# Kernel optimization log

Measured on AMD Instinct MI355X. Metric: run time of the kernel, lower is better.

## Reference

```python
import jax, jax.numpy as jnp
import numpy as np

S = 3000    # number of candidate spans (rows of g_i)
P = 80000   # total (mention, antecedent) pairs
GI = 768    # gi_dim
DD = 20     # distance/genre/speaker embedding dim
HID = 150   # mlp hidden dim (fixed in source)
ORDER = 2   # N: one higher-order refinement pass


def setup_inputs() -> dict:
    key = jax.random.key(0)
    ks = jax.random.split(key, 18)
    gij = 3 * GI + 3 * DD
    g_i = jax.random.normal(ks[0], (S, GI), jnp.float32)
    mention_scores = jax.random.normal(ks[1], (S, 1), jnp.float32)
    # sorted segment ids: ragged antecedent counts per mention, grouped contiguously
    mention_ids = jnp.sort(jax.random.randint(ks[2], (P,), 0, S, dtype=jnp.int32))
    antecedent_ids = jax.random.randint(ks[3], (P,), 0, S, dtype=jnp.int32)
    dist_bins = jax.random.randint(ks[4], (P,), 0, 10, dtype=jnp.int32)
    genre_ids = jax.random.randint(ks[5], (P,), 0, 7, dtype=jnp.int32) + 1   # 1..7, 0 is padding_idx
    speaker_ids = jax.random.randint(ks[6], (P,), 0, 2, dtype=jnp.int32) + 1  # 1..2, 0 is padding_idx
    w = lambda k, shp: 0.02 * jax.random.normal(k, shp, jnp.float32)
    dist_emb = w(ks[7], (10, DD))
    genre_emb = w(ks[8], (8, DD)).at[0].set(0.0)     # padding_idx=0
    speaker_emb = w(ks[9], (3, DD)).at[0].set(0.0)   # padding_idx=0
    W1 = w(ks[10], (gij, HID)); b1 = jnp.zeros((HID,), jnp.float32)
    W2 = w(ks[11], (HID, HID)); b2 = jnp.zeros((HID,), jnp.float32)
    W3 = w(ks[12], (HID, 1)); b3 = jnp.zeros((1,), jnp.float32)
    Wf = w(ks[13], (2 * GI, 1)); bf = jnp.zeros((1,), jnp.float32)
    return {"g_i": g_i, "mention_scores": mention_scores, "mention_ids": mention_ids,
            "antecedent_ids": antecedent_ids, "dist_bins": dist_bins, "genre_ids": genre_ids,
            "speaker_ids": speaker_ids, "dist_emb": dist_emb, "genre_emb": genre_emb,
            "speaker_emb": speaker_emb, "W1": W1, "b1": b1, "W2": W2, "b2": b2,
            "W3": W3, "b3": b3, "Wf": Wf, "bf": bf}


def _mlp(x, W1, b1, W2, b2, W3, b3):
    h = jax.nn.relu(x @ W1 + b1)
    h = jax.nn.relu(h @ W2 + b2)
    return h @ W3 + b3


def reference(g_i, mention_scores, mention_ids, antecedent_ids, dist_bins, genre_ids,
              speaker_ids, dist_emb, genre_emb, speaker_emb, W1, b1, W2, b2, W3, b3, Wf, bf):
    phi = jnp.concatenate([dist_emb[dist_bins], genre_emb[genre_ids], speaker_emb[speaker_ids]], axis=1)  # [P,60]
    seg = dict(num_segments=S, indices_are_sorted=True)
    g = g_i
    scores = None
    for n in range(ORDER):
        i_g = g[mention_ids]                # [P,GI] gather
        j_g = g[antecedent_ids]             # [P,GI] gather
        pairs = jnp.concatenate([i_g, j_g, i_g * j_g, phi], axis=1)  # [P,gij]
        scores = _mlp(pairs, W1, b1, W2, b2, W3, b3)                 # [P,1]
        if n < ORDER - 1:
            # higher_order_refinement: ragged segment softmax + weighted scatter update
            s = scores[:, 0]
            seg_max = jax.ops.segment_max(s, mention_ids, **seg)
            safe_max = jnp.where(jnp.isfinite(seg_max), seg_max, 0.0)
            e = jnp.exp(s - safe_max[mention_ids])
            denom = jax.ops.segment_sum(e, mention_ids, **seg)
            attn = e / jnp.where(denom > 0, denom, 1.0)[mention_ids]
            weighted = jax.ops.segment_sum(attn[:, None] * j_g, mention_ids, **seg)  # [S,GI]
            counts = jax.ops.segment_sum(jnp.ones_like(s), mention_ids, **seg)
            f = jax.nn.sigmoid(jnp.concatenate([g, weighted], axis=1) @ Wf + bf)  # [S,1]
            # NOTE: faithful to the source bug: f * mention_id (the integer index), not f * mention_g
            ids_f = jnp.arange(S, dtype=g.dtype)[:, None]
            g_new = f * ids_f + (1.0 - f) * weighted
            g = jnp.where(counts[:, None] > 0, g_new, g)
    s_i = mention_scores[mention_ids]
    s_j = mention_scores[antecedent_ids]
    coref_scores = s_i + s_j + scores       # [P,1]
    # segment softmax with an extra epsilon (score 0) logit per mention
    c = coref_scores[:, 0]
    seg_max = jax.ops.segment_max(c, mention_ids, **seg)
    m = jnp.maximum(jnp.where(jnp.isfinite(seg_max), seg_max, 0.0), 0.0)  # include epsilon logit 0
    e = jnp.exp(c - m[mention_ids])
    denom = jax.ops.segment_sum(e, mention_ids, **seg) + jnp.exp(-m)
    pair_probs = e / denom[mention_ids]     # [P]
    eps_probs = jnp.exp(-m) / denom         # [S]
    return coref_scores, pair_probs, eps_probs
```

## Files before the change

kernel.cpp:

```cpp
#include <hip/hip_runtime.h>

#define GI   768
#define HID  150
#define HPAD 160
#define DDIM 20

typedef __attribute__((ext_vector_type(8))) short v8s;
typedef __attribute__((ext_vector_type(4))) float f32x4;

#define MFMA16(A, B, C) __builtin_amdgcn_mfma_f32_16x16x32_bf16(A, B, C, 0, 0, 0)

__device__ __forceinline__ ushort bf16rn(float x) {
  unsigned u = __float_as_uint(x);
  return (ushort)((u + 0x7fffu + ((u >> 16) & 1u)) >> 16);
}
__device__ __forceinline__ float b2f(ushort u) {
  return __uint_as_float((unsigned)u << 16);
}
__device__ __forceinline__ void tsplit(float x, ushort& h, ushort& l) {
  unsigned u = __float_as_uint(x);
  h = (ushort)(u >> 16);
  float d = x - __uint_as_float(u & 0xffff0000u);
  l = (ushort)(__float_as_uint(d) >> 16);
}
__device__ __forceinline__ uint4 pack8(const ushort* v) {
  uint4 r;
  r.x = v[0] | ((unsigned)v[1] << 16); r.y = v[2] | ((unsigned)v[3] << 16);
  r.z = v[4] | ((unsigned)v[5] << 16); r.w = v[6] | ((unsigned)v[7] << 16);
  return r;
}
__device__ __forceinline__ v8s mk8(const ushort* v) {
  union { uint4 u; v8s s; } t;
  t.u = pack8(v);
  return t.s;
}

__global__ void seg_kernel(const int* __restrict__ mI, int* __restrict__ segs,
                           int P, int S) {
  int m = blockIdx.x * 256 + threadIdx.x;
  if (m > S) return;
  int lo = 0, hi = P;
  while (lo < hi) { int mid = (lo + hi) >> 1; if (mI[mid] < m) lo = mid + 1; else hi = mid; }
  segs[m] = lo;
}

__global__ void phi_kernel(const float* __restrict__ de, const float* __restrict__ ge,
                           const float* __restrict__ se, const float* __restrict__ W1,
                           float* __restrict__ phiW) {
  int idx = blockIdx.x * 256 + threadIdx.x;
  if (idx >= 21 * HPAD) return;
  int row = idx / HPAD, h = idx % HPAD;
  float v = 0.f;
  if (h < HID) {
    const float* emb; int off;
    if (row < 10)      { emb = de + row * DDIM;        off = 0; }
    else if (row < 18) { emb = ge + (row - 10) * DDIM; off = DDIM; }
    else               { emb = se + (row - 18) * DDIM; off = 2 * DDIM; }
    for (int k = 0; k < DDIM; ++k) v += emb[k] * W1[(3 * GI + off + k) * HID + h];
  }
  phiW[row * HPAD + h] = v;
}

__global__ void g2b_kernel(const float* __restrict__ g, ushort* __restrict__ gb, int n4) {
  int i = blockIdx.x * 256 + threadIdx.x;
  if (i >= n4) return;
  const float4 v = *(const float4*)(g + 4 * (size_t)i);
  ushort4 o;
  o.x = bf16rn(v.x); o.y = bf16rn(v.y); o.z = bf16rn(v.z); o.w = bf16rn(v.w);
  *(ushort4*)(gb + 4 * (size_t)i) = o;
}

#define NWC  (10 * 24 * 512)
#define NW16 (20 * 24 * 512)
#define NW2C (10 * 5 * 512)
__global__ void pad2_kernel(const float* __restrict__ W1, const float* __restrict__ W2,
                            const float* __restrict__ b1, const float* __restrict__ b2,
                            const float* __restrict__ W3,
                            ushort* __restrict__ WC, ushort* __restrict__ W16,
                            ushort* __restrict__ W2Chi, ushort* __restrict__ W2Clo,
                            float* __restrict__ b1p, float2* __restrict__ b2w3) {
  int idx = blockIdx.x * 256 + threadIdx.x;
  if (idx < NWC) {
    int ct = idx / (24 * 512); int r1 = idx % (24 * 512);
    int s = r1 / 512; int r2 = r1 % 512;
    int l = r2 / 8, j = r2 % 8;
    int col = ct * 16 + (l & 15);
    int k = s * 32 + 8 * (l >> 4) + j;
    float x = (col < HID) ? W1[(size_t)(2 * GI + k) * HID + col] : 0.f;
    WC[idx] = bf16rn(x); return;
  }
  idx -= NWC;
  if (idx < NW16) {
    int ct = idx / (24 * 512); int r1 = idx % (24 * 512);
    int s = r1 / 512; int r2 = r1 % 512;
    int l = r2 / 8, j = r2 % 8;
    int col = ct * 16 + (l & 15);
    int k = s * 32 + 8 * (l >> 4) + j;
    int seg = col / HPAD, h = col % HPAD;
    float x = (h < HID) ? W1[(size_t)(seg * GI + k) * HID + h] : 0.f;
    W16[idx] = bf16rn(x); return;
  }
  idx -= NW16;
  if (idx < NW2C) {
    int ct = idx / (5 * 512); int r1 = idx % (5 * 512);
    int s = r1 / 512; int r2 = r1 % 512;
    int l = r2 / 8, j = r2 % 8;
    int col = ct * 16 + (l & 15);
    int k = s * 32 + 8 * (l >> 4) + j;
    float x = (k < HID && col < HID) ? W2[(size_t)k * HID + col] : 0.f;
    ushort hh = bf16rn(x);
    float lo = x - __uint_as_float((unsigned)hh << 16);
    W2Chi[idx] = hh; W2Clo[idx] = bf16rn(lo); return;
  }
  idx -= NW2C;
  if (idx < HPAD) { b1p[idx] = (idx < HID) ? b1[idx] : 0.f; return; }
  idx -= HPAD;
  if (idx < HPAD) {
    b2w3[idx] = make_float2((idx < HID) ? b2[idx] : 0.f, (idx < HID) ? W3[idx] : 0.f);
    return;
  }
}

__global__ __launch_bounds__(64, 4) void pre3_kernel(
    const float* __restrict__ g, const ushort* __restrict__ W16,
    ushort* __restrict__ preb, int S) {
  const int lane = threadIdx.x;
  const int ct = blockIdx.x;
  const int row0 = blockIdx.y * 16;
  int srow = row0 + (lane & 15); if (srow >= S) srow = S - 1;
  const float* gp = g + (size_t)srow * GI + 8 * (lane >> 4);
  const ushort* wp = W16 + ((size_t)ct * 24 * 64 + lane) * 8;

  f32x4 acc = {};
#pragma unroll 2
  for (int s = 0; s < 24; ++s) {
    const float4 a0 = *(const float4*)(gp + s * 32);
    const float4 a1 = *(const float4*)(gp + s * 32 + 4);
    const v8s bh = *(const v8s*)(wp + (size_t)s * 512);
    float xr[8] = {a0.x, a0.y, a0.z, a0.w, a1.x, a1.y, a1.z, a1.w};
    ushort hs[8], ls[8];
#pragma unroll
    for (int j = 0; j < 8; ++j) tsplit(xr[j], hs[j], ls[j]);
    const v8s ah = mk8(hs), al = mk8(ls);
    acc = MFMA16(ah, bh, acc);
    acc = MFMA16(al, bh, acc);
  }
  const int col = ct * 16 + (lane & 15);
#pragma unroll
  for (int r = 0; r < 4; ++r) {
    int sr = row0 + (lane >> 4) * 4 + r;
    if (sr < S) preb[(size_t)sr * 320 + col] = bf16rn(acc[r]);
  }
}

template<bool BF16G>
__global__ __launch_bounds__(64, 4) void h1s_kernel(
    const float* __restrict__ g, const ushort* __restrict__ gb,
    const ushort* __restrict__ preb, const float* __restrict__ phiW,
    const ushort* __restrict__ WC,
    const ushort* __restrict__ W2Chi, const ushort* __restrict__ W2Clo,
    const float* __restrict__ b1p, const float2* __restrict__ b2w3,
    const float* __restrict__ b3,
    const int* __restrict__ mI, const int* __restrict__ aI,
    const int* __restrict__ db, const int* __restrict__ ge,
    const int* __restrict__ sp,
    float* __restrict__ sOut, int P) {
  __shared__ ushort h1L[16 * 160];
  const int lane = threadIdx.x;
  const int lrow = lane & 15, kg = lane >> 4;
  const int p0 = blockIdx.x * 16;
  const int myp = p0 + lrow;
  const int iA = mI[myp], jA = aI[myp];
  const int rdL = db[myp], rgL = 10 + ge[myp], rsL = 18 + sp[myp];

  f32x4 acc[10];
  {
    f32x4 z = {};
#pragma unroll
    for (int c = 0; c < 10; ++c) acc[c] = z;
  }

  if constexpr (BF16G) {
    const ushort* gbi = gb + (size_t)iA * GI + 8 * kg;
    const ushort* gbj = gb + (size_t)jA * GI + 8 * kg;
#pragma unroll 2
    for (int s = 0; s < 24; ++s) {
      const int d0 = s * 32;
      const v8s ai = *(const v8s*)(gbi + d0);
      const v8s aj = *(const v8s*)(gbj + d0);
      ushort pr[8];
#pragma unroll
      for (int j = 0; j < 8; ++j)
        pr[j] = bf16rn(b2f((ushort)ai[j]) * b2f((ushort)aj[j]));
      const v8s ap = mk8(pr);
#pragma unroll
      for (int c = 0; c < 10; ++c) {
        const v8s w = *(const v8s*)(WC + ((size_t)(c * 24 + s) * 64 + lane) * 8);
        acc[c] = MFMA16(ap, w, acc[c]);
      }
    }
  } else {
    const float* gi = g + (size_t)iA * GI + 8 * kg;
    const float* gj = g + (size_t)jA * GI + 8 * kg;
#pragma unroll 2
    for (int s = 0; s < 24; ++s) {
      const int d0 = s * 32;
      const float4 a0 = *(const float4*)(gi + d0);
      const float4 a1 = *(const float4*)(gi + d0 + 4);
      const float4 b0 = *(const float4*)(gj + d0);
      const float4 b1v = *(const float4*)(gj + d0 + 4);
      float xr[8] = {a0.x * b0.x, a0.y * b0.y, a0.z * b0.z, a0.w * b0.w,
                     a1.x * b1v.x, a1.y * b1v.y, a1.z * b1v.z, a1.w * b1v.w};
      ushort hs[8], ls[8];
#pragma unroll
      for (int j = 0; j < 8; ++j) tsplit(xr[j], hs[j], ls[j]);
      const v8s ah = mk8(hs), al = mk8(ls);
#pragma unroll
      for (int c = 0; c < 10; ++c) {
        const v8s w = *(const v8s*)(WC + ((size_t)(c * 24 + s) * 64 + lane) * 8);
        acc[c] = MFMA16(ah, w, acc[c]);
        acc[c] = MFMA16(al, w, acc[c]);
      }
    }
  }

#pragma unroll
  for (int r = 0; r < 4; ++r) {
    const int p = kg * 4 + r;
    const int pI = __shfl(iA, p);
    const int pJ = __shfl(jA, p);
    const int rd = __shfl(rdL, p), rg = __shfl(rgL, p), rs = __shfl(rsL, p);
    const ushort* prI = preb + (size_t)pI * 320;
    const ushort* prJ = preb + (size_t)pJ * 320 + 160;
#pragma unroll
    for (int c = 0; c < 10; ++c) {
      const int col = c * 16 + lrow;
      float v = acc[c][r] + b1p[col] + b2f(prI[col]) + b2f(prJ[col])
              + phiW[rd * HPAD + col] + phiW[rg * HPAD + col] + phiW[rs * HPAD + col];
      v = fmaxf(v, 0.f);
      h1L[p * 160 + col] = bf16rn(v);
    }
  }
  __syncthreads();

  f32x4 acc2[10];
  {
    f32x4 z = {};
#pragma unroll
    for (int ct = 0; ct < 10; ++ct) acc2[ct] = z;
  }
#pragma unroll
  for (int s = 0; s < 5; ++s) {
    const v8s a = *(const v8s*)(&h1L[lrow * 160 + s * 32 + 8 * kg]);
#pragma unroll
    for (int ct = 0; ct < 10; ++ct) {
      const size_t o = ((size_t)(ct * 5 + s) * 64 + lane) * 8;
      const v8s wh = *(const v8s*)(W2Chi + o);
      const v8s wl = *(const v8s*)(W2Clo + o);
      acc2[ct] = MFMA16(a, wh, acc2[ct]);
      acc2[ct] = MFMA16(a, wl, acc2[ct]);
    }
  }
  float part[4] = {0.f, 0.f, 0.f, 0.f};
#pragma unroll
  for (int ct = 0; ct < 10; ++ct) {
    const float2 bw = b2w3[ct * 16 + lrow];
#pragma unroll
    for (int r = 0; r < 4; ++r)
      part[r] += fmaxf(acc2[ct][r] + bw.x, 0.f) * bw.y;
  }
#pragma unroll
  for (int m = 1; m < 16; m <<= 1) {
#pragma unroll
    for (int r = 0; r < 4; ++r) part[r] += __shfl_xor(part[r], m, 16);
  }
  if (lrow == 0) {
    const float bb = b3[0];
#pragma unroll
    for (int r = 0; r < 4; ++r) sOut[p0 + kg * 4 + r] = part[r] + bb;
  }
}

__global__ void mid_kernel(const float* __restrict__ g, const ushort* __restrict__ gb,
                           const float* __restrict__ s1,
                           const int* __restrict__ segs, const int* __restrict__ aI,
                           const float* __restrict__ Wf, const float* __restrict__ bf,
                           float* __restrict__ g2) {
  const int m = blockIdx.x;
  const int t = threadIdx.x;
  const int st = segs[m], en = segs[m + 1], n = en - st;
  if (n == 0) {
    for (int d = t; d < GI; d += 256) g2[m * GI + d] = g[m * GI + d];
    return;
  }
  __shared__ float red[256];
  __shared__ float wred[4][GI];
  float mx = -INFINITY;
  for (int p = st + t; p < en; p += 256) mx = fmaxf(mx, s1[p]);
  red[t] = mx; __syncthreads();
  for (int s = 128; s > 0; s >>= 1) { if (t < s) red[t] = fmaxf(red[t], red[t + s]); __syncthreads(); }
  mx = red[0]; __syncthreads();
  const int dg = t & 63, pg = t >> 6;
  float wv[12];
#pragma unroll
  for (int u = 0; u < 12; ++u) wv[u] = 0.f;
  float esum = 0.f;
  for (int p = st + pg; p < en; p += 4) {
    const float e = expf(s1[p] - mx);
    esum += e;
    const ushort* gj = gb + (size_t)aI[p] * GI + dg;
#pragma unroll
    for (int u = 0; u < 12; ++u) wv[u] += e * b2f(gj[u * 64]);
  }
  red[t] = (dg == 0) ? esum : 0.f; __syncthreads();
  for (int s = 128; s > 0; s >>= 1) { if (t < s) red[t] += red[t + s]; __syncthreads(); }
  const float denom = red[0]; __syncthreads();
#pragma unroll
  for (int u = 0; u < 12; ++u) wred[pg][dg + u * 64] = wv[u];
  __syncthreads();
  float part = 0.f;
  float wfin[3];
#pragma unroll
  for (int u = 0; u < 3; ++u) {
    const int d = t + u * 256;
    float wsv = (wred[0][d] + wred[1][d] + wred[2][d] + wred[3][d]) / denom;
    wfin[u] = wsv;
    part += g[(size_t)m * GI + d] * Wf[d] + wsv * Wf[GI + d];
  }
  red[t] = part; __syncthreads();
  for (int s = 128; s > 0; s >>= 1) { if (t < s) red[t] += red[t + s]; __syncthreads(); }
  const float f = 1.f / (1.f + expf(-(red[0] + bf[0])));
#pragma unroll
  for (int u = 0; u < 3; ++u) {
    const int d = t + u * 256;
    g2[(size_t)m * GI + d] = f * (float)m + (1.f - f) * wfin[u];
  }
}

__global__ void coref_kernel(const float* __restrict__ ms, const float* __restrict__ s2,
                             const int* __restrict__ mI, const int* __restrict__ aI,
                             float* __restrict__ out, int P) {
  int p = blockIdx.x * 256 + threadIdx.x;
  if (p >= P) return;
  out[p] = ms[mI[p]] + ms[aI[p]] + s2[p];
}

__global__ void final_kernel(const float* __restrict__ c, const int* __restrict__ segs,
                             float* __restrict__ pairP, float* __restrict__ epsP) {
  const int m = blockIdx.x;
  const int t = threadIdx.x;
  const int st = segs[m], en = segs[m + 1], n = en - st;
  __shared__ float red[256];
  float mx = -INFINITY;
  for (int p = st + t; p < en; p += 256) mx = fmaxf(mx, c[p]);
  red[t] = mx; __syncthreads();
  for (int s = 128; s > 0; s >>= 1) { if (t < s) red[t] = fmaxf(red[t], red[t + s]); __syncthreads(); }
  mx = red[0]; __syncthreads();
  const float m2 = (n > 0) ? fmaxf(mx, 0.f) : 0.f;
  float sm = 0.f;
  for (int p = st + t; p < en; p += 256) sm += expf(c[p] - m2);
  red[t] = sm; __syncthreads();
  for (int s = 128; s > 0; s >>= 1) { if (t < s) red[t] += red[t + s]; __syncthreads(); }
  const float denom = red[0] + expf(-m2);
  for (int p = st + t; p < en; p += 256) pairP[p] = expf(c[p] - m2) / denom;
  if (t == 0) epsP[m] = expf(-m2) / denom;
}

extern "C" void kernel_launch(void* const* d_in, const int* in_sizes, int n_in,
                              void* d_out, int out_size, void* d_ws, size_t ws_size,
                              hipStream_t stream) {
  const float* g_i  = (const float*)d_in[0];
  const float* ms   = (const float*)d_in[1];
  const int*   mI   = (const int*)d_in[2];
  const int*   aI   = (const int*)d_in[3];
  const int*   db   = (const int*)d_in[4];
  const int*   ge   = (const int*)d_in[5];
  const int*   sp   = (const int*)d_in[6];
  const float* de   = (const float*)d_in[7];
  const float* gemb = (const float*)d_in[8];
  const float* semb = (const float*)d_in[9];
  const float* W1   = (const float*)d_in[10];
  const float* b1   = (const float*)d_in[11];
  const float* W2   = (const float*)d_in[12];
  const float* b2   = (const float*)d_in[13];
  const float* W3   = (const float*)d_in[14];
  const float* b3   = (const float*)d_in[15];
  const float* Wf   = (const float*)d_in[16];
  const float* bf   = (const float*)d_in[17];

  const int S = in_sizes[0] / GI;
  const int P = in_sizes[2];
  float* out = (float*)d_out;

  char* ws = (char*)d_ws;
  size_t off = 0;
  auto take = [&](size_t bytes) -> char* {
    char* p = ws + off;
    off = (off + bytes + 15) & ~(size_t)15;
    return p;
  };
  int*    segs  = (int*)   take((size_t)(S + 1) * 4);
  float*  phiW  = (float*) take((size_t)21 * HPAD * 4);
  ushort* preb  = (ushort*)take((size_t)S * 320 * 2);
  float*  g2    = (float*) take((size_t)S * GI * 4);
  float*  s1    = (float*) take((size_t)P * 4);
  float*  s2    = (float*) take((size_t)P * 4);
  ushort* Gb    = (ushort*)take((size_t)S * GI * 2);
  ushort* WC    = (ushort*)take((size_t)NWC * 2);
  ushort* W16   = (ushort*)take((size_t)NW16 * 2);
  ushort* W2Chi = (ushort*)take((size_t)NW2C * 2);
  ushort* W2Clo = (ushort*)take((size_t)NW2C * 2);
  float*  b1p   = (float*) take((size_t)HPAD * 4);
  float2* b2w3  = (float2*)take((size_t)HPAD * 8);

  const int gridSeg = (S + 1 + 255) / 256;
  const int gridPhi = (21 * HPAD + 255) / 256;
  const int padTot  = NWC + NW16 + NW2C + 2 * HPAD;
  const int gridPad = (padTot + 255) / 256;
  const int n4      = S * GI / 4;
  const int gridGb  = (n4 + 255) / 256;
  const dim3 gridPre(20, (S + 15) / 16);
  const int gridH   = P / 16;
  const int gridCor = (P + 255) / 256;

  seg_kernel<<<gridSeg, 256, 0, stream>>>(mI, segs, P, S);
  phi_kernel<<<gridPhi, 256, 0, stream>>>(de, gemb, semb, W1, phiW);
  pad2_kernel<<<gridPad, 256, 0, stream>>>(W1, W2, b1, b2, W3, WC, W16,
                                           W2Chi, W2Clo, b1p, b2w3);
  g2b_kernel<<<gridGb, 256, 0, stream>>>(g_i, Gb, n4);

  pre3_kernel<<<gridPre, 64, 0, stream>>>(g_i, W16, preb, S);
  h1s_kernel<true><<<gridH, 64, 0, stream>>>(g_i, Gb, preb, phiW, WC, W2Chi, W2Clo,
                                             b1p, b2w3, b3, mI, aI, db, ge, sp, s1, P);
  mid_kernel<<<S, 256, 0, stream>>>(g_i, Gb, s1, segs, aI, Wf, bf, g2);

  pre3_kernel<<<gridPre, 64, 0, stream>>>(g2, W16, preb, S);
  h1s_kernel<false><<<gridH, 64, 0, stream>>>(g2, Gb, preb, phiW, WC, W2Chi, W2Clo,
                                              b1p, b2w3, b3, mI, aI, db, ge, sp, s2, P);

  coref_kernel<<<gridCor, 256, 0, stream>>>(ms, s2, mI, aI, out, P);
  final_kernel<<<S, 256, 0, stream>>>(out, segs, out + P, out + 2 * (size_t)P);
}
```

Before: 447.8 us.

## Split pair-product gather into a separate A-build kernel feeding a dense MFMA kernel

Adds an abuild kernel that gathers g_i*g_j products per pair and writes them, already split into bf16 hi/lo parts, into a pre-swizzled workspace laid out for MFMA A operands. A new h1dense kernel then streams those tiles with contiguous loads instead of doing scattered gathers and conversions inside the MLP kernel. The dense path is used only when the workspace is large enough, and it adds roughly 2x80000x768x2 bytes of writes and reads per pass.

```diff
diff --git a/kernel.cpp b/kernel.cpp
--- a/kernel.cpp
+++ b/kernel.cpp
@@ -150,6 +150,180 @@
   for (int r = 0; r < 4; ++r) {
     int sr = row0 + (lane >> 4) * 4 + r;
     if (sr < S) preb[(size_t)sr * 320 + col] = bf16rn(acc[r]);
+  }
+}
+
+template<bool BF16G>
+__global__ __launch_bounds__(256, 4) void abuild_kernel(
+    const float* __restrict__ g, const ushort* __restrict__ gb,
+    const int* __restrict__ mI, const int* __restrict__ aI,
+    ushort* __restrict__ Ahi, ushort* __restrict__ Alo, int P) {
+  const int lane = threadIdx.x & 63;
+  const int w = threadIdx.x >> 6;
+  const int t = blockIdx.x * 4 + w;
+  const int pbase = t * 16;
+
+#pragma unroll 2
+  for (int q = 0; q < 16; ++q) {
+    const int p = pbase + q;
+    const int iA = mI[p], jA = aI[p];
+    if constexpr (BF16G) {
+      const ushort* gi = gb + (size_t)iA * GI;
+      const ushort* gj = gb + (size_t)jA * GI;
+      const uint4 ia = *(const uint4*)(gi + lane * 8);
+      const uint4 ja = *(const uint4*)(gj + lane * 8);
+      uint4 ib = {}, jb = {};
+      if (lane < 32) {
+        ib = *(const uint4*)(gi + 512 + lane * 8);
+        jb = *(const uint4*)(gj + 512 + lane * 8);
+      }
+      {
+        const ushort* iap = (const ushort*)&ia;
+        const ushort* jap = (const ushort*)&ja;
+        ushort pa[8];
+#pragma unroll
+        for (int j = 0; j < 8; ++j) pa[j] = bf16rn(b2f(iap[j]) * b2f(jap[j]));
+        const size_t oA = (((size_t)t * 24 + (lane >> 2)) * 64 + (q + 16 * (lane & 3))) * 8;
+        *(uint4*)(Ahi + oA) = pack8(pa);
+      }
+      if (lane < 32) {
+        const ushort* ibp = (const ushort*)&ib;
+        const ushort* jbp = (const ushort*)&jb;
+        ushort pb[8];
+#pragma unroll
+        for (int j = 0; j < 8; ++j) pb[j] = bf16rn(b2f(ibp[j]) * b2f(jbp[j]));
+        const size_t oB = (((size_t)t * 24 + 16 + (lane >> 2)) * 64 + (q + 16 * (lane & 3))) * 8;
+        *(uint4*)(Ahi + oB) = pack8(pb);
+      }
+    } else {
+      const float* gi = g + (size_t)iA * GI;
+      const float* gj = g + (size_t)jA * GI;
+#pragma unroll
+      for (int c = 0; c < 3; ++c) {
+        const float4 a = *(const float4*)(gi + c * 256 + lane * 4);
+        const float4 b = *(const float4*)(gj + c * 256 + lane * 4);
+        const float pr[4] = {a.x * b.x, a.y * b.y, a.z * b.z, a.w * b.w};
+        ushort hs[4], ls[4];
+#pragma unroll
+        for (int j = 0; j < 4; ++j) tsplit(pr[j], hs[j], ls[j]);
+        const int s = c * 8 + (lane >> 3);
+        const int kg = (lane & 7) >> 1;
+        const size_t o = (((size_t)t * 24 + s) * 64 + (q + 16 * kg)) * 8 + (lane & 1) * 4;
+        uint2 ph, pl;
+        ph.x = hs[0] | ((unsigned)hs[1] << 16); ph.y = hs[2] | ((unsigned)hs[3] << 16);
+        pl.x = ls[0] | ((unsigned)ls[1] << 16); pl.y = ls[2] | ((unsigned)ls[3] << 16);
+        *(uint2*)(Ahi + o) = ph;
+        *(uint2*)(Alo + o) = pl;
+      }
+    }
+  }
+}
+
+template<bool BF16G>
+__global__ __launch_bounds__(64, 4) void h1dense_kernel(
+    const ushort* __restrict__ Ahi, const ushort* __restrict__ Alo,
+    const ushort* __restrict__ preb, const float* __restrict__ phiW,
+    const ushort* __restrict__ WC,
+    const ushort* __restrict__ W2Chi, const ushort* __restrict__ W2Clo,
+    const float* __restrict__ b1p, const float2* __restrict__ b2w3,
+    const float* __restrict__ b3,
+    const int* __restrict__ mI, const int* __restrict__ aI,
+    const int* __restrict__ db, const int* __restrict__ ge,
+    const int* __restrict__ sp,
+    float* __restrict__ sOut, int P) {
+  __shared__ ushort h1L[16 * 160];
+  const int lane = threadIdx.x;
+  const int lrow = lane & 15, kg = lane >> 4;
+  const int t = blockIdx.x;
+  const int p0 = t * 16;
+  const int myp = p0 + lrow;
+  const int iA = mI[myp], jA = aI[myp];
+  const int rdL = db[myp], rgL = 10 + ge[myp], rsL = 18 + sp[myp];
+
+  f32x4 acc[10];
+  {
+    f32x4 z = {};
+#pragma unroll
+    for (int c = 0; c < 10; ++c) acc[c] = z;
+  }
+
+  const ushort* Ah = Ahi + ((size_t)t * 24 * 64 + lane) * 8;
+#pragma unroll 2
+  for (int s = 0; s < 24; ++s) {
+    if constexpr (BF16G) {
+      const v8s a = *(const v8s*)(Ah + (size_t)s * 512);
+#pragma unroll
+      for (int c = 0; c < 10; ++c) {
+        const v8s w = *(const v8s*)(WC + ((size_t)(c * 24 + s) * 64 + lane) * 8);
+        acc[c] = MFMA16(a, w, acc[c]);
+      }
+    } else {
+      const ushort* Al = Alo + ((size_t)t * 24 * 64 + lane) * 8;
+      const v8s ah = *(const v8s*)(Ah + (size_t)s * 512);
+      const v8s al = *(const v8s*)(Al + (size_t)s * 512);
+#pragma unroll
+      for (int c = 0; c < 10; ++c) {
+        const v8s w = *(const v8s*)(WC + ((size_t)(c * 24 + s) * 64 + lane) * 8);
+        acc[c] = MFMA16(ah, w, acc[c]);
+        acc[c] = MFMA16(al, w, acc[c]);
+      }
+    }
+  }
+
+#pragma unroll
+  for (int r = 0; r < 4; ++r) {
+    const int p = kg * 4 + r;
+    const int pI = __shfl(iA, p);
+    const int pJ = __shfl(jA, p);
+    const int rd = __shfl(rdL, p), rg = __shfl(rgL, p), rs = __shfl(rsL, p);
+    const ushort* prI = preb + (size_t)pI * 320;
+    const ushort* prJ = preb + (size_t)pJ * 320 + 160;
+#pragma unroll
+    for (int c = 0; c < 10; ++c) {
+      const int col = c * 16 + lrow;
+      float v = acc[c][r] + b1p[col] + b2f(prI[col]) + b2f(prJ[col])
+              + phiW[rd * HPAD + col] + phiW[rg * HPAD + col] + phiW[rs * HPAD + col];
+      v = fmaxf(v, 0.f);
+      h1L[p * 160 + col] = bf16rn(v);
+    }
+  }
+  __syncthreads();
+
+  f32x4 acc2[10];
+  {
+    f32x4 z = {};
+#pragma unroll
+    for (int ct = 0; ct < 10; ++ct) acc2[ct] = z;
+  }
+#pragma unroll
+  for (int s = 0; s < 5; ++s) {
+    const v8s a = *(const v8s*)(&h1L[lrow * 160 + s * 32 + 8 * kg]);
+#pragma unroll
+    for (int ct = 0; ct < 10; ++ct) {
+      const size_t o = ((size_t)(ct * 5 + s) * 64 + lane) * 8;
+      const v8s wh = *(const v8s*)(W2Chi + o);
+      const v8s wl = *(const v8s*)(W2Clo + o);
+      acc2[ct] = MFMA16(a, wh, acc2[ct]);
+      acc2[ct] = MFMA16(a, wl, acc2[ct]);
+    }
+  }
+  float part[4] = {0.f, 0.f, 0.f, 0.f};
+#pragma unroll
+  for (int ct = 0; ct < 10; ++ct) {
+    const float2 bw = b2w3[ct * 16 + lrow];
+#pragma unroll
+    for (int r = 0; r < 4; ++r)
+      part[r] += fmaxf(acc2[ct][r] + bw.x, 0.f) * bw.y;
+  }
+#pragma unroll
+  for (int m = 1; m < 16; m <<= 1) {
+#pragma unroll
+    for (int r = 0; r < 4; ++r) part[r] += __shfl_xor(part[r], m, 16);
+  }
+  if (lrow == 0) {
+    const float bb = b3[0];
+#pragma unroll
+    for (int r = 0; r < 4; ++r) sOut[p0 + kg * 4 + r] = part[r] + bb;
   }
 }
 
@@ -413,6 +587,15 @@
   float*  b1p   = (float*) take((size_t)HPAD * 4);
   float2* b2w3  = (float2*)take((size_t)HPAD * 8);
 
+  const int NT = P / 16;
+  const size_t aBytes = (size_t)NT * 24 * 512 * 2;
+  const bool dense = (ws_size >= off + 2 * aBytes + 256);
+  ushort* Ahi = nullptr; ushort* Alo = nullptr;
+  if (dense) {
+    Ahi = (ushort*)take(aBytes);
+    Alo = (ushort*)take(aBytes);
+  }
+
   const int gridSeg = (S + 1 + 255) / 256;
   const int gridPhi = (21 * HPAD + 255) / 256;
   const int padTot  = NWC + NW16 + NW2C + 2 * HPAD;
@@ -420,7 +603,8 @@
   const int n4      = S * GI / 4;
   const int gridGb  = (n4 + 255) / 256;
   const dim3 gridPre(20, (S + 15) / 16);
-  const int gridH   = P / 16;
+  const int gridH   = NT;
+  const int gridAB  = NT / 4;
   const int gridCor = (P + 255) / 256;
 
   seg_kernel<<<gridSeg, 256, 0, stream>>>(mI, segs, P, S);
@@ -430,13 +614,27 @@
   g2b_kernel<<<gridGb, 256, 0, stream>>>(g_i, Gb, n4);
 
   pre3_kernel<<<gridPre, 64, 0, stream>>>(g_i, W16, preb, S);
-  h1s_kernel<true><<<gridH, 64, 0, stream>>>(g_i, Gb, preb, phiW, WC, W2Chi, W2Clo,
-                                             b1p, b2w3, b3, mI, aI, db, ge, sp, s1, P);
+  if (dense) {
+    abuild_kernel<true><<<gridAB, 256, 0, stream>>>(g_i, Gb, mI, aI, Ahi, Alo, P);
+    h1dense_kernel<true><<<gridH, 64, 0, stream>>>(Ahi, Alo, preb, phiW, WC,
+                                                   W2Chi, W2Clo, b1p, b2w3, b3,
+                                                   mI, aI, db, ge, sp, s1, P);
+  } else {
+    h1s_kernel<true><<<gridH, 64, 0, stream>>>(g_i, Gb, preb, phiW, WC, W2Chi, W2Clo,
+                                               b1p, b2w3, b3, mI, aI, db, ge, sp, s1, P);
+  }
   mid_kernel<<<S, 256, 0, stream>>>(g_i, Gb, s1, segs, aI, Wf, bf, g2);
 
   pre3_kernel<<<gridPre, 64, 0, stream>>>(g2, W16, preb, S);
-  h1s_kernel<false><<<gridH, 64, 0, stream>>>(g2, Gb, preb, phiW, WC, W2Chi, W2Clo,
-                                              b1p, b2w3, b3, mI, aI, db, ge, sp, s2, P);
+  if (dense) {
+    abuild_kernel<false><<<gridAB, 256, 0, stream>>>(g2, Gb, mI, aI, Ahi, Alo, P);
+    h1dense_kernel<false><<<gridH, 64, 0, stream>>>(Ahi, Alo, preb, phiW, WC,
+                                                    W2Chi, W2Clo, b1p, b2w3, b3,
+                                                    mI, aI, db, ge, sp, s2, P);
+  } else {
+    h1s_kernel<false><<<gridH, 64, 0, stream>>>(g2, Gb, preb, phiW, WC, W2Chi, W2Clo,
+                                                b1p, b2w3, b3, mI, aI, db, ge, sp, s2, P);
+  }
 
   coref_kernel<<<gridCor, 256, 0, stream>>>(ms, s2, mI, aI, out, P);
   final_kernel<<<S, 256, 0, stream>>>(out, segs, out + P, out + 2 * (size_t)P);
```

Measured after the change: 673.9 us. 50.5% more time.
